# Optimization experiments

Hardware: AMD Instinct MI355X
Metric: run time of the kernel (lower is better)

Reference implementation:

```python
import jax, jax.numpy as jnp
import numpy as np

B, P, T, R, A = 16384, 3, 2, 3, 3   # batch, n_players, teammates, rivals, action_dim
HID = [1024, 512]
ENC_OUT = 64
RIVAL_START = 9 * 9 + 12 * P       # 117, as in the torch module
NEG_SLOPE = 0.01                    # nn.LeakyReLU default


def _linpack(key, k, din, dout):
    # PyTorch nn.Linear default init: U(-1/sqrt(din), 1/sqrt(din))
    kw, kb = jax.random.split(key)
    bound = 1.0 / np.sqrt(din)
    W = jax.random.uniform(kw, (k, din, dout), jnp.float32, -bound, bound)
    b = jax.random.uniform(kb, (k, dout), jnp.float32, -bound, bound)
    return W, b


def setup_inputs() -> dict:
    key = jax.random.key(0)
    ks = jax.random.split(key, 16)
    obs = jax.random.normal(ks[0], (B, P, 144), jnp.float32)
    act = jax.random.normal(ks[1], (B, P, A), jnp.float32)
    # stacked per-segment encoder weights (grouped small GEMMs)
    Wp1, bp1 = _linpack(ks[2], 9, 2 + A, 32)
    Wp2, bp2 = _linpack(ks[3], 9, 32, ENC_OUT)
    Wt1, bt1 = _linpack(ks[4], T, 12, 32)
    Wt2, bt2 = _linpack(ks[5], T, 32, ENC_OUT)
    Wr1, br1 = _linpack(ks[6], R, 9, 32)
    Wr2, br2 = _linpack(ks[7], R, 32, ENC_OUT)
    # q head: [P*896] -> 1024 -> 512 -> P
    din = P * (9 + T + R) * ENC_OUT
    Wq1, bq1 = _linpack(ks[8], 1, din, HID[0]);  Wq1, bq1 = Wq1[0], bq1[0]
    Wq2, bq2 = _linpack(ks[9], 1, HID[0], HID[1]); Wq2, bq2 = Wq2[0], bq2[0]
    Wq3, bq3 = _linpack(ks[10], 1, HID[1], P);   Wq3, bq3 = Wq3[0], bq3[0]
    return dict(obs=obs, act=act,
                Wp1=Wp1, bp1=bp1, Wp2=Wp2, bp2=bp2,
                Wt1=Wt1, bt1=bt1, Wt2=Wt2, bt2=bt2,
                Wr1=Wr1, br1=br1, Wr2=Wr2, br2=br2,
                Wq1=Wq1, bq1=bq1, Wq2=Wq2, bq2=bq2, Wq3=Wq3, bq3=bq3)


def _enc2(x, W1, b1, W2, b2):
    # x: [B, P, K, din]; W1: [K, din, 32]; W2: [K, 32, 64] -> [B, P, K, 64]
    lrelu = lambda v: jax.nn.leaky_relu(v, NEG_SLOPE)
    h = lrelu(jnp.einsum('bpki,kio->bpko', x, W1) + b1)
    return lrelu(jnp.einsum('bpkh,kho->bpko', h, W2) + b2)


def reference(obs, act, Wp1, bp1, Wp2, bp2, Wt1, bt1, Wt2, bt2,
              Wr1, br1, Wr2, br2, Wq1, bq1, Wq2, bq2, Wq3, bq3):
    b = obs.shape[0]
    # prop segments: obs[:, :, 2i:2i+2] concat act  -> [B, P, 9, 2+A]
    x_prop = jnp.concatenate(
        [obs[:, :, :18].reshape(b, P, 9, 2),
         jnp.broadcast_to(act[:, :, None, :], (b, P, 9, A))], axis=-1)
    x_team = obs[:, :, 18:18 + 12 * T].reshape(b, P, T, 12)
    x_riv = obs[:, :, RIVAL_START:RIVAL_START + 9 * R].reshape(b, P, R, 9)
    ep = _enc2(x_prop, Wp1, bp1, Wp2, bp2)   # [B, P, 9, 64]
    et = _enc2(x_team, Wt1, bt1, Wt2, bt2)   # [B, P, T, 64]
    er = _enc2(x_riv, Wr1, br1, Wr2, br2)    # [B, P, R, 64]
    enc = jnp.concatenate([ep, et, er], axis=2).reshape(b, -1)  # [B, P*14*64]
    # q head: ReLU hidden activations, identity output
    h = jax.nn.relu(enc @ Wq1 + bq1)
    h = jax.nn.relu(h @ Wq2 + bq2)
    return h @ Wq3 + bq3                      # [B, P]
```

## Files before the change

### kernel.cpp

```cpp
#include <hip/hip_runtime.h>
#include <hip/hip_bf16.h>
#include <cstdint>

typedef __bf16 bf16x8 __attribute__((ext_vector_type(8)));
typedef float f32x4 __attribute__((ext_vector_type(4)));

__device__ __forceinline__ void gld16(const __bf16* g, __bf16* lds) {
    __builtin_amdgcn_global_load_lds(
        (__attribute__((address_space(1))) void*)(uintptr_t)g,
        (__attribute__((address_space(3))) void*)(uint32_t)(uintptr_t)lds,
        16, 0, 0);
}

__global__ __launch_bounds__(256) void transpose_bf16_k(const float* __restrict__ in,
                                                        __bf16* __restrict__ out,
                                                        int R, int C) {
    __shared__ float t[64][65];
    const int r0 = blockIdx.x * 64, c0 = blockIdx.y * 64;
    const int tid = threadIdx.x;
#pragma unroll
    for (int i = 0; i < 16; i++) {
        int idx = i * 256 + tid;
        int rr = idx >> 6, cc = idx & 63;
        t[rr][cc] = in[(size_t)(r0 + rr) * C + (c0 + cc)];
    }
    __syncthreads();
#pragma unroll
    for (int i = 0; i < 16; i++) {
        int idx = i * 256 + tid;
        int rr = idx >> 6, cc = idx & 63;
        out[(size_t)(c0 + rr) * R + (r0 + cc)] = (__bf16)t[cc][rr];
    }
}

__global__ __launch_bounds__(256) void pack_weights(const float* __restrict__ Wp1, const float* __restrict__ bp1,
                                                    const float* __restrict__ Wp2, const float* __restrict__ bp2,
                                                    const float* __restrict__ Wt1, const float* __restrict__ bt1,
                                                    const float* __restrict__ Wt2, const float* __restrict__ bt2,
                                                    const float* __restrict__ Wr1, const float* __restrict__ br1,
                                                    const float* __restrict__ Wr2, const float* __restrict__ br2,
                                                    float* __restrict__ w1p, __bf16* __restrict__ w2t) {
    const int s = blockIdx.x, tid = threadIdx.x;
    int ks, din, w1off;
    const float *W1, *B1, *W2, *B2;
    if (s < 9)      { ks = s;      din = 5;  w1off = s * 160;
                      W1 = Wp1; B1 = bp1; W2 = Wp2; B2 = bp2; }
    else if (s < 11){ ks = s - 9;  din = 12; w1off = 1440 + ks * 384;
                      W1 = Wt1; B1 = bt1; W2 = Wt2; B2 = bt2; }
    else            { ks = s - 11; din = 9;  w1off = 2208 + ks * 288;
                      W1 = Wr1; B1 = br1; W2 = Wr2; B2 = br2; }
    W1 += ks * din * 32; B1 += ks * 32; W2 += ks * 2048; B2 += ks * 64;
    for (int i = tid; i < din * 32; i += 256) w1p[w1off + i] = W1[i];
    if (tid < 32) w1p[3072 + s * 32 + tid] = B1[tid];
    if (tid < 64) w1p[3520 + s * 64 + tid] = B2[tid];
    for (int i = tid; i < 2048; i += 256) {
        const int o = i >> 5, k = i & 31;
        w2t[s * 2048 + i] = (__bf16)W2[k * 64 + o];
    }
}

__global__ __launch_bounds__(192) void enc_fused(const float* __restrict__ obs,
                                                 const float* __restrict__ act,
                                                 const float* __restrict__ w1p,
                                                 const __bf16* __restrict__ w2t,
                                                 __bf16* __restrict__ enc) {
    __shared__ float sW[4416];
    __shared__ __bf16 sH[2][192 * 40];
    const int tid = threadIdx.x;
    for (int i = tid; i < 4416; i += 192) sW[i] = w1p[i];
    const int row = blockIdx.x * 192 + tid;
    const float* orow = obs + (size_t)row * 144;
    const float a0 = act[row * 3], a1 = act[row * 3 + 1], a2 = act[row * 3 + 2];
    const int wv = tid >> 6, lane = tid & 63;
    const int fr = lane & 15, kq = lane >> 4;
    const int rq = (lane >> 4) << 2;
    __syncthreads();
    int buf = 0;

    auto l2 = [&](int s) {
        __syncthreads();
        bf16x8 bfr[4], afr[4];
#pragma unroll
        for (int n = 0; n < 4; n++)
            bfr[n] = *(const bf16x8*)&w2t[(s * 64 + n * 16 + fr) * 32 + kq * 8];
#pragma unroll
        for (int m = 0; m < 4; m++)
            afr[m] = *(const bf16x8*)&sH[buf][(wv * 64 + m * 16 + fr) * 40 + kq * 8];
        f32x4 acc[4][4] = {};
#pragma unroll
        for (int m = 0; m < 4; m++)
#pragma unroll
            for (int n = 0; n < 4; n++)
                acc[m][n] = __builtin_amdgcn_mfma_f32_16x16x32_bf16(afr[m], bfr[n], acc[m][n], 0, 0, 0);
        const float* b2 = sW + 3520 + s * 64;
#pragma unroll
        for (int m = 0; m < 4; m++) {
            const size_t rG = (size_t)blockIdx.x * 192 + wv * 64 + m * 16 + rq;
#pragma unroll
            for (int n = 0; n < 4; n++) {
                const float bv = b2[n * 16 + fr];
#pragma unroll
                for (int rg = 0; rg < 4; rg++) {
                    float v = acc[m][n][rg] + bv;
                    v = fmaxf(v, 0.01f * v);
                    enc[(rG + rg) * 896 + s * 64 + n * 16 + fr] = (__bf16)v;
                }
            }
        }
        buf ^= 1;
    };

#define L1(DIN, W1OFF, SGI, XLOAD)                                   \
    {                                                                \
        float x[DIN];                                                \
        XLOAD;                                                       \
        const float* w1 = sW + (W1OFF);                              \
        const float* b1 = sW + 3072 + (SGI) * 32;                    \
        float h[32];                                                 \
        _Pragma("unroll") for (int o = 0; o < 32; o++) {             \
            float a_ = b1[o];                                        \
            _Pragma("unroll") for (int i = 0; i < DIN; i++)          \
                a_ += x[i] * w1[i * 32 + o];                         \
            h[o] = fmaxf(a_, 0.01f * a_);                            \
        }                                                            \
        __bf16* hr = &sH[buf][tid * 40];                             \
        _Pragma("unroll") for (int sl = 0; sl < 4; sl++) {           \
            bf16x8 t_;                                               \
            _Pragma("unroll") for (int j = 0; j < 8; j++)            \
                t_[j] = (__bf16)h[sl * 8 + j];                       \
            *(bf16x8*)&hr[sl * 8] = t_;                              \
        }                                                            \
    }

    for (int k = 0; k < 9; k++) {
        L1(5, k * 160, k,
           { x[0] = orow[2 * k]; x[1] = orow[2 * k + 1]; x[2] = a0; x[3] = a1; x[4] = a2; })
        l2(k);
    }
    for (int k = 0; k < 2; k++) {
        L1(12, 1440 + k * 384, 9 + k,
           { _Pragma("unroll") for (int i = 0; i < 12; i++) x[i] = orow[18 + 12 * k + i]; })
        l2(9 + k);
    }
    for (int k = 0; k < 3; k++) {
        L1(9, 2208 + k * 288, 11 + k,
           { _Pragma("unroll") for (int i = 0; i < 9; i++) x[i] = orow[117 + 9 * k + i]; })
        l2(11 + k);
    }
#undef L1
}

template <int NB>
__global__ __launch_bounds__(512, 2) void gemm256_relu(const __bf16* __restrict__ Ag,
                                                       const __bf16* __restrict__ Btg,
                                                       const float* __restrict__ bias,
                                                       __bf16* __restrict__ Cg,
                                                       int N, int K, int lgn) {
    __shared__ __align__(16) __bf16 ldsA[2][2][128 * 64];
    __shared__ __align__(16) __bf16 ldsB[2][2][NB * 64 * 64];
    const int tid = threadIdx.x;
    const int wid = tid >> 6, lane = tid & 63;
    const int wm = wid >> 2, wn = wid & 3;
    const int fr = lane & 15, kq = lane >> 4;

    const int chunk = gridDim.x >> 3;
    const int wg = (blockIdx.x & 7) * chunk + (blockIdx.x >> 3);
    const int bn = wg & ((1 << lgn) - 1), bm = wg >> lgn;

    const int c0 = tid, c1 = tid + 512;
    const int r0 = c0 >> 3, s0 = (c0 & 7) ^ (r0 & 7);
    const int r1 = c1 >> 3, s1 = (c1 & 7) ^ (r1 & 7);
    const size_t aH = (size_t)128 * K;
    const size_t bH = (size_t)(NB * 64) * K;
    const __bf16* aB0 = Ag + (size_t)(bm * 256 + r0) * K + s0 * 8;
    const __bf16* aB1 = Ag + (size_t)(bm * 256 + r1) * K + s1 * 8;
    const __bf16* bB0 = Btg + (size_t)(bn * (NB * 128) + r0) * K + s0 * 8;
    const __bf16* bB1 = Btg + (size_t)(bn * (NB * 128) + r1) * K + s1 * 8;

    f32x4 acc[2][2][4][NB] = {};
    bf16x8 a0[4][2], a1[4][2], b0[NB][2], b1[NB][2];

#define STAGE_A(BUF, H, KO)                                   \
    do {                                                      \
        __bf16* d_ = &ldsA[BUF][H][0];                        \
        gld16(aB0 + (H)*aH + (KO), d_ + c0 * 8);              \
        gld16(aB1 + (H)*aH + (KO), d_ + c1 * 8);              \
    } while (0)
#define STAGE_B(BUF, H, KO)                                   \
    do {                                                      \
        __bf16* d_ = &ldsB[BUF][H][0];                        \
        gld16(bB0 + (H)*bH + (KO), d_ + c0 * 8);              \
        if constexpr (NB == 2) gld16(bB1 + (H)*bH + (KO), d_ + c1 * 8); \
    } while (0)

#define LDFA(BUF, H, ROW, KS) \
    (*(const bf16x8*)&ldsA[BUF][H][(ROW) * 64 + ((((KS)*4 + kq) ^ ((ROW)&7)) * 8)])
#define LDFB(BUF, H, ROW, KS) \
    (*(const bf16x8*)&ldsB[BUF][H][(ROW) * 64 + ((((KS)*4 + kq) ^ ((ROW)&7)) * 8)])

#define LOAD_A(BUF, H, DST)                                   \
    _Pragma("unroll") for (int m = 0; m < 4; m++)             \
        _Pragma("unroll") for (int ks = 0; ks < 2; ks++)      \
            DST[m][ks] = LDFA(BUF, H, wm * 64 + m * 16 + fr, ks);
#define LOAD_B(BUF, H, DST)                                   \
    _Pragma("unroll") for (int n = 0; n < NB; n++)            \
        _Pragma("unroll") for (int ks = 0; ks < 2; ks++)      \
            DST[n][ks] = LDFB(BUF, H, wn * (NB * 16) + n * 16 + fr, ks);

#define MM(Q, R, AR, BR)                                      \
    __builtin_amdgcn_s_setprio(1);                            \
    _Pragma("unroll") for (int ks = 0; ks < 2; ks++)          \
        _Pragma("unroll") for (int m = 0; m < 4; m++)         \
            _Pragma("unroll") for (int n = 0; n < NB; n++)    \
                acc[Q][R][m][n] = __builtin_amdgcn_mfma_f32_16x16x32_bf16( \
                    AR[m][ks], BR[n][ks], acc[Q][R][m][n], 0, 0, 0); \
    __builtin_amdgcn_s_setprio(0);

#define SB0 __builtin_amdgcn_sched_barrier(0)
#define BAR __builtin_amdgcn_s_barrier()
#define LGKM_B1                                               \
    if constexpr (NB == 2) asm volatile("s_waitcnt lgkmcnt(4)" ::: "memory"); \
    else asm volatile("s_waitcnt lgkmcnt(2)" ::: "memory");
#define LGKM(NSTR) asm volatile("s_waitcnt lgkmcnt(" NSTR ")" ::: "memory")
#define VMW0 asm volatile("s_waitcnt vmcnt(0)" ::: "memory")

    const int NT = K >> 6;

    STAGE_A(0, 0, 0);
    STAGE_B(0, 0, 0);
    STAGE_B(0, 1, 0);
    STAGE_A(0, 1, 0);
    VMW0;
    BAR;
    LOAD_A(0, 0, a0)
    LOAD_B(0, 0, b0)
    SB0;

    for (int t = 0; t < NT; ++t) {
        const int buf = t & 1, nb = buf ^ 1;
        const int kO = (t + 1) << 6;
        const bool st = (t + 1 < NT);

        LOAD_B(buf, 1, b1)
        if (st) {
            STAGE_A(nb, 0, kO);
            STAGE_B(nb, 0, kO);
            STAGE_B(nb, 1, kO);
            STAGE_A(nb, 1, kO);
        }
        SB0;
        BAR;
        LGKM_B1;
        SB0;
        MM(0, 0, a0, b0)

        LOAD_A(buf, 1, a1)
        SB0;
        BAR;
        LGKM("8");
        SB0;
        MM(0, 1, a0, b1)

        BAR;
        LGKM("0");
        SB0;
        MM(1, 0, a1, b0)

        VMW0;
        BAR;
        if (st) {
            LOAD_A(nb, 0, a0)
            LOAD_B(nb, 0, b0)
        }
        SB0;
        MM(1, 1, a1, b1)
    }

    const int cc = lane & 15, rr = (lane >> 4) << 2;
#pragma unroll
    for (int q = 0; q < 2; q++)
#pragma unroll
        for (int r2 = 0; r2 < 2; r2++)
#pragma unroll
            for (int m = 0; m < 4; m++)
#pragma unroll
                for (int n = 0; n < NB; n++) {
                    const int colG = bn * (NB * 128) + r2 * (NB * 64) + wn * (NB * 16) + n * 16 + cc;
                    const int rowG = bm * 256 + q * 128 + wm * 64 + m * 16 + rr;
                    const float bv = bias[colG];
#pragma unroll
                    for (int reg = 0; reg < 4; reg++) {
                        float v = acc[q][r2][m][n][reg] + bv;
                        v = fmaxf(v, 0.0f);
                        Cg[(size_t)(rowG + reg) * N + colG] = (__bf16)v;
                    }
                }
#undef STAGE_A
#undef STAGE_B
#undef LDFA
#undef LDFB
#undef LOAD_A
#undef LOAD_B
#undef MM
#undef SB0
#undef BAR
#undef LGKM_B1
#undef LGKM
#undef VMW0
}

__global__ __launch_bounds__(256) void head_kernel(const __bf16* __restrict__ h2,
                                                   const float* __restrict__ Wq3,
                                                   const float* __restrict__ bq3,
                                                   float* __restrict__ out) {
    const int wave = threadIdx.x >> 6, lane = threadIdx.x & 63;
    const int row = blockIdx.x * 4 + wave;
    const bf16x8 hv = *(const bf16x8*)(h2 + (size_t)row * 512 + lane * 8);
    float s0 = 0.f, s1 = 0.f, s2 = 0.f;
#pragma unroll
    for (int i = 0; i < 8; i++) {
        const float hf = (float)hv[i];
        const int k = lane * 8 + i;
        s0 += hf * Wq3[k * 3 + 0];
        s1 += hf * Wq3[k * 3 + 1];
        s2 += hf * Wq3[k * 3 + 2];
    }
#pragma unroll
    for (int off = 32; off > 0; off >>= 1) {
        s0 += __shfl_xor(s0, off);
        s1 += __shfl_xor(s1, off);
        s2 += __shfl_xor(s2, off);
    }
    if (lane == 0) {
        float* o = out + (size_t)row * 3;
        o[0] = s0 + bq3[0];
        o[1] = s1 + bq3[1];
        o[2] = s2 + bq3[2];
    }
}

extern "C" void kernel_launch(void* const* d_in, const int* in_sizes, int n_in,
                              void* d_out, int out_size, void* d_ws, size_t ws_size,
                              hipStream_t stream) {
    const float* obs = (const float*)d_in[0];
    const float* act = (const float*)d_in[1];
    const float* Wp1 = (const float*)d_in[2];  const float* bp1 = (const float*)d_in[3];
    const float* Wp2 = (const float*)d_in[4];  const float* bp2 = (const float*)d_in[5];
    const float* Wt1 = (const float*)d_in[6];  const float* bt1 = (const float*)d_in[7];
    const float* Wt2 = (const float*)d_in[8];  const float* bt2 = (const float*)d_in[9];
    const float* Wr1 = (const float*)d_in[10]; const float* br1 = (const float*)d_in[11];
    const float* Wr2 = (const float*)d_in[12]; const float* br2 = (const float*)d_in[13];
    const float* Wq1 = (const float*)d_in[14]; const float* bq1 = (const float*)d_in[15];
    const float* Wq2 = (const float*)d_in[16]; const float* bq2 = (const float*)d_in[17];
    const float* Wq3 = (const float*)d_in[18]; const float* bq3 = (const float*)d_in[19];
    float* out = (float*)d_out;

    char* ws = (char*)d_ws;
    __bf16* enc = (__bf16*)(ws);
    __bf16* h1  = (__bf16*)(ws + 88080384);
    __bf16* h2  = (__bf16*)(ws + 88080384 + 33554432);
    __bf16* w1t = (__bf16*)(ws + 138412032);
    __bf16* w2t = (__bf16*)(ws + 143917056);
    float*  w1p = (float*)(ws + 144965632);
    __bf16* w2e = (__bf16*)(ws + 144983296);

    pack_weights<<<14, 256, 0, stream>>>(Wp1, bp1, Wp2, bp2, Wt1, bt1, Wt2, bt2,
                                         Wr1, br1, Wr2, br2, w1p, w2e);
    transpose_bf16_k<<<dim3(2688 / 64, 1024 / 64), 256, 0, stream>>>(Wq1, w1t, 2688, 1024);
    transpose_bf16_k<<<dim3(1024 / 64, 512 / 64), 256, 0, stream>>>(Wq2, w2t, 1024, 512);

    enc_fused<<<256, 192, 0, stream>>>(obs, act, w1p, w2e, enc);

    gemm256_relu<2><<<dim3(256), 512, 0, stream>>>(enc, w1t, bq1, h1, 1024, 2688, 2);
    gemm256_relu<1><<<dim3(256), 512, 0, stream>>>(h1, w2t, bq2, h2, 512, 1024, 2);
    head_kernel<<<16384 / 4, 256, 0, stream>>>(h2, Wq3, bq3, out);
}
```

Measured before the change: 167.5 us.

## Split global staging across MFMA phases with partial vmcnt waits and peeled tail

The GEMM main loop now issues the next tile's global-to-LDS staging in two halves placed around the first MFMA phase, and waits on partial vmcnt counts instead of draining all outstanding loads. The last K iteration is peeled out so the loop body carries no stage-or-not branch. The goal is to overlap more of the global memory latency with MFMA work and cut full-drain stalls. The risk is that the hand-counted vmcnt values are wrong for the real number of loads per stage, which would cause LDS races that produce silently wrong results.

```diff
diff --git a/kernel.cpp b/kernel.cpp
--- a/kernel.cpp
+++ b/kernel.cpp
@@ -222,7 +222,9 @@
     if constexpr (NB == 2) asm volatile("s_waitcnt lgkmcnt(4)" ::: "memory"); \
     else asm volatile("s_waitcnt lgkmcnt(2)" ::: "memory");
 #define LGKM(NSTR) asm volatile("s_waitcnt lgkmcnt(" NSTR ")" ::: "memory")
-#define VMW0 asm volatile("s_waitcnt vmcnt(0)" ::: "memory")
+#define VMW(NSTR) asm volatile("s_waitcnt vmcnt(" NSTR ")" ::: "memory")
+#define VMW2(N2, N1)                                          \
+    if constexpr (NB == 2) VMW(#N2); else VMW(#N1);
 
     const int NT = K >> 6;
 
@@ -230,30 +232,28 @@
     STAGE_B(0, 0, 0);
     STAGE_B(0, 1, 0);
     STAGE_A(0, 1, 0);
-    VMW0;
+    VMW("2");
     BAR;
     LOAD_A(0, 0, a0)
     LOAD_B(0, 0, b0)
     SB0;
 
-    for (int t = 0; t < NT; ++t) {
+    for (int t = 0; t < NT - 1; ++t) {
         const int buf = t & 1, nb = buf ^ 1;
         const int kO = (t + 1) << 6;
-        const bool st = (t + 1 < NT);
-
+
+        STAGE_A(nb, 0, kO);
+        STAGE_B(nb, 0, kO);
+        VMW2(4, 3);
         LOAD_B(buf, 1, b1)
-        if (st) {
-            STAGE_A(nb, 0, kO);
-            STAGE_B(nb, 0, kO);
-            STAGE_B(nb, 1, kO);
-            STAGE_A(nb, 1, kO);
-        }
         SB0;
         BAR;
         LGKM_B1;
         SB0;
         MM(0, 0, a0, b0)
 
+        STAGE_B(nb, 1, kO);
+        STAGE_A(nb, 1, kO);
         LOAD_A(buf, 1, a1)
         SB0;
         BAR;
@@ -266,13 +266,36 @@
         SB0;
         MM(1, 0, a1, b0)
 
-        VMW0;
-        BAR;
-        if (st) {
-            LOAD_A(nb, 0, a0)
-            LOAD_B(nb, 0, b0)
-        }
-        SB0;
+        VMW("2");
+        BAR;
+        LOAD_A(nb, 0, a0)
+        LOAD_B(nb, 0, b0)
+        SB0;
+        MM(1, 1, a1, b1)
+    }
+
+    {
+        const int buf = (NT - 1) & 1;
+        VMW("0");
+        LOAD_B(buf, 1, b1)
+        SB0;
+        BAR;
+        LGKM_B1;
+        SB0;
+        MM(0, 0, a0, b0)
+
+        LOAD_A(buf, 1, a1)
+        SB0;
+        BAR;
+        LGKM("8");
+        SB0;
+        MM(0, 1, a0, b1)
+
+        BAR;
+        LGKM("0");
+        SB0;
+        MM(1, 0, a1, b0)
+
         MM(1, 1, a1, b1)
     }
 
@@ -306,7 +329,8 @@
 #undef BAR
 #undef LGKM_B1
 #undef LGKM
-#undef VMW0
+#undef VMW
+#undef VMW2
 }
 
 __global__ __launch_bounds__(256) void head_kernel(const __bf16* __restrict__ h2,
```

Result: faster. 162.0 us (-3.3%).
